# Kernel tuning notes

Measured on AMD Instinct MI355X. Metric: run time of the kernel, lower is better.

The kernel has to match this reference:

```python
import jax, jax.numpy as jnp
import numpy as np

GAMMA = 0.99


def setup_inputs() -> dict:
    key = jax.random.key(0)
    ks = jax.random.split(key, 6)
    T, D, H = 65536, 1024, 1024
    s1 = 1.0 / np.sqrt(D)
    s2 = 1.0 / np.sqrt(H)
    return {
        "rewards": jax.random.normal(ks[0], (T,), jnp.float32),
        "obs": jax.random.normal(ks[1], (T, D), jnp.float32),
        "W1": jax.random.normal(ks[2], (D, H), jnp.float32) * s1,
        "b1": jnp.zeros((H,), jnp.float32),
        "W2": jax.random.normal(ks[3], (H, H), jnp.float32) * s2,
        "b2": jnp.zeros((H,), jnp.float32),
        "W3": jax.random.normal(ks[4], (H, 1), jnp.float32) * s2,
        "b3": jnp.zeros((1,), jnp.float32),
    }


def _discounted_returns(rewards):
    # G[i] = r[i] + gamma * G[i+1], computed as a reverse scan
    def step(g, r):
        g = r + GAMMA * g
        return g, g
    _, G = jax.lax.scan(step, jnp.zeros((), rewards.dtype), rewards, reverse=True)
    return G


def reference(rewards, obs, W1, b1, W2, b2, W3, b3):
    G = _discounted_returns(rewards)              # [T]
    h = jax.nn.relu(obs @ W1 + b1)                # [T, H]
    h = jax.nn.relu(h @ W2 + b2)                  # [T, H]
    V = (h @ W3 + b3).reshape(-1)                 # [T]
    return G - V
```

## Files before the change

kernel.cpp:

```cpp
#include <hip/hip_runtime.h>

typedef __bf16 bf16x8 __attribute__((ext_vector_type(8)));
typedef __bf16 bf16x4 __attribute__((ext_vector_type(4)));
typedef float  f32x4  __attribute__((ext_vector_type(4)));

#define GAMMA 0.99f

__device__ __forceinline__ void gload_lds16(const void* g, void* l) {
  __builtin_amdgcn_global_load_lds(
      (const __attribute__((address_space(1))) void*)g,
      (__attribute__((address_space(3))) void*)l, 16, 0, 0);
}

#define VMCNT(n) asm volatile("s_waitcnt vmcnt(" #n ")" ::: "memory")
#define BAR() __builtin_amdgcn_s_barrier()
#define MFMA(d, a, b) d = __builtin_amdgcn_mfma_f32_16x16x32_bf16(a, b, d, 0, 0, 0)

__global__ __launch_bounds__(1024) void prep(
    const float* __restrict__ rw, float* __restrict__ G,
    const float* __restrict__ W1, const float* __restrict__ W2,
    __bf16* __restrict__ BT1, __bf16* __restrict__ BT2) {
  __shared__ float smem[4224];
  const int blk = blockIdx.x;
  const int t = threadIdx.x;
  if (blk == 0) {
    float* sv = smem;
    const float4* rp = (const float4*)(rw + t * 64);
    float4 lv[16];
#pragma unroll
    for (int i = 0; i < 16; ++i) lv[i] = rp[i];
    float loc[64];
#pragma unroll
    for (int i = 0; i < 16; ++i) {
      loc[4 * i + 0] = lv[i].x; loc[4 * i + 1] = lv[i].y;
      loc[4 * i + 2] = lv[i].z; loc[4 * i + 3] = lv[i].w;
    }
    float g = 0.f;
#pragma unroll
    for (int j = 63; j >= 0; --j) { g = loc[j] + GAMMA * g; loc[j] = g; }
    sv[t] = g;
    float W = GAMMA;
#pragma unroll
    for (int i = 0; i < 6; ++i) W *= W;
    float v = g;
    for (int s = 1; s < 1024; s <<= 1) {
      __syncthreads();
      float o = (t + s < 1024) ? sv[t + s] : 0.f;
      __syncthreads();
      v += W * o;
      sv[t] = v;
      W *= W;
    }
    __syncthreads();
    const float nxt = (t < 1023) ? sv[t + 1] : 0.f;
    float pw = GAMMA;
#pragma unroll
    for (int j = 63; j >= 0; --j) {
      G[t * 64 + j] = loc[j] + pw * nxt;
      pw *= GAMMA;
    }
  } else {
    const int sub = t >> 8, tt = t & 255;
    const int wi = (blk - 1) * 4 + sub;
    const float* W = (wi >= 1024) ? W2 : W1;
    __bf16* O = (wi >= 1024) ? BT2 : BT1;
    const int tile = wi & 1023;
    const int ti = tile >> 5, tj = tile & 31;
    float* s = smem + sub * 1056;
    const int rr = tt >> 3, c4 = (tt & 7) * 4;
    float4 v = *(const float4*)(W + (size_t)(ti * 32 + rr) * 1024 + tj * 32 + c4);
    s[rr * 33 + c4 + 0] = v.x; s[rr * 33 + c4 + 1] = v.y;
    s[rr * 33 + c4 + 2] = v.z; s[rr * 33 + c4 + 3] = v.w;
    __syncthreads();
    bf16x4 o = {(__bf16)s[(c4 + 0) * 33 + rr], (__bf16)s[(c4 + 1) * 33 + rr],
                (__bf16)s[(c4 + 2) * 33 + rr], (__bf16)s[(c4 + 3) * 33 + rr]};
    *(bf16x4*)(O + (size_t)(tj * 32 + rr) * 1024 + ti * 32 + c4) = o;
  }
}

__global__ __launch_bounds__(512, 2) void gemm1(
    const float* __restrict__ obs, const __bf16* __restrict__ BT1,
    const float* __restrict__ b1, __bf16* __restrict__ h1) {
  extern __shared__ char lds[];
  const int t = threadIdx.x, lane = t & 63, w = t >> 6;
  const int wsr = w >> 2, wsc = w & 3, g = lane >> 4, l15 = lane & 15;
  const int bid = blockIdx.x;
  const int mb = (bid & 7) * 32 + ((bid >> 3) >> 2);
  const int nb = (bid >> 3) & 3;

  const size_t stg_off =
      (size_t)(t >> 2) * 2048 + (size_t)(((t & 3) ^ ((t >> 3) & 3)) * 16);
  const char* Bg = (const char*)BT1 + (size_t)nb * 524288 + stg_off;
  const char* Asrc = (const char*)obs +
      ((size_t)(mb * 256 + w * 32 + (lane >> 3)) * 4096) +
      (size_t)(16 * ((lane & 7) ^ (lane >> 3)));
  const int aldst = w * 4096 + lane * 16;

  const int csw = (g ^ ((l15 >> 1) & 3)) << 4;
  const int brb = (wsc * 32 + l15) * 64 + csw;

  f32x4 acc[2][4][2][2];
  const f32x4 zero = {0.f, 0.f, 0.f, 0.f};
#pragma unroll
  for (int a_ = 0; a_ < 2; ++a_)
#pragma unroll
    for (int b_ = 0; b_ < 4; ++b_)
#pragma unroll
      for (int c_ = 0; c_ < 2; ++c_)
#pragma unroll
        for (int d_ = 0; d_ < 2; ++d_) acc[a_][b_][c_][d_] = zero;

  auto STA = [&](int buf, int kt) {
    const char* s = Asrc + kt * 128;
    char* d = lds + buf * 49152 + aldst;
    gload_lds16(s, d);
    gload_lds16(s + 32768, d + 1024);
    gload_lds16(s + 65536, d + 2048);
    gload_lds16(s + 98304, d + 3072);
  };
  auto STB = [&](int buf, int kt) {
    const char* s = Bg + kt * 64;
    char* d = lds + buf * 49152 + 32768 + t * 16;
    gload_lds16(s, d);
    gload_lds16(s + 262144, d + 8192);
  };
  auto LDAF = [&](const char* ab, int r) -> bf16x8 {
    const int o1 = (g * 32) ^ ((r & 7) << 4);
    const f32x4 a0 = *(const f32x4*)(ab + r * 128 + o1);
    const f32x4 a1 = *(const f32x4*)(ab + r * 128 + (o1 ^ 16));
    bf16x8 v = {(__bf16)a0[0], (__bf16)a0[1], (__bf16)a0[2], (__bf16)a0[3],
                (__bf16)a1[0], (__bf16)a1[1], (__bf16)a1[2], (__bf16)a1[3]};
    return v;
  };
  auto COMPUTE = [&](int bc) {
    const char* ab = lds + bc * 49152;
    const char* bb = ab + 32768;
    bf16x8 bfr[2][2], afr[4];
#pragma unroll
    for (int nh = 0; nh < 2; ++nh)
#pragma unroll
      for (int j = 0; j < 2; ++j)
        bfr[nh][j] = *(const bf16x8*)(bb + brb + (nh * 128 + j * 16) * 64);
#pragma unroll
    for (int i = 0; i < 4; ++i) afr[i] = LDAF(ab, wsr * 64 + 16 * i + l15);
    __builtin_amdgcn_s_setprio(1);
#pragma unroll
    for (int i = 0; i < 4; ++i)
#pragma unroll
      for (int nh = 0; nh < 2; ++nh)
#pragma unroll
        for (int j = 0; j < 2; ++j)
          MFMA(acc[0][i][nh][j], bfr[nh][j], afr[i]);
    __builtin_amdgcn_s_setprio(0);
#pragma unroll
    for (int i = 0; i < 4; ++i)
      afr[i] = LDAF(ab, 128 + wsr * 64 + 16 * i + l15);
    __builtin_amdgcn_s_setprio(1);
#pragma unroll
    for (int i = 0; i < 4; ++i)
#pragma unroll
      for (int nh = 0; nh < 2; ++nh)
#pragma unroll
        for (int j = 0; j < 2; ++j)
          MFMA(acc[1][i][nh][j], bfr[nh][j], afr[i]);
    __builtin_amdgcn_s_setprio(0);
  };

  STA(0, 0); STB(0, 0);
  STA(1, 1); STB(1, 1);
  int bc = 0;
  for (int kt = 0; kt < 30; ++kt) {
    int bs = bc + 2; if (bs >= 3) bs -= 3;
    STA(bs, kt + 2);
    STB(bs, kt + 2);
    VMCNT(12);
    BAR();
    COMPUTE(bc);
    BAR();
    bc = bc + 1; if (bc >= 3) bc -= 3;
  }
  VMCNT(6);
  BAR();
  COMPUTE(bc);
  BAR();
  bc = bc + 1; if (bc >= 3) bc -= 3;
  VMCNT(0);
  BAR();
  COMPUTE(bc);

  f32x4 b1q[2][2];
#pragma unroll
  for (int nh = 0; nh < 2; ++nh)
#pragma unroll
    for (int j = 0; j < 2; ++j)
      b1q[nh][j] =
          *(const f32x4*)(b1 + nb * 256 + nh * 128 + wsc * 32 + j * 16 + g * 4);
#pragma unroll
  for (int mh = 0; mh < 2; ++mh)
#pragma unroll
    for (int i = 0; i < 4; ++i) {
      const size_t mrow = (size_t)(mb * 256 + mh * 128 + wsr * 64 + i * 16 + l15);
#pragma unroll
      for (int nh = 0; nh < 2; ++nh)
#pragma unroll
        for (int j = 0; j < 2; ++j) {
          f32x4 v = acc[mh][i][nh][j];
          v.x += b1q[nh][j].x; v.y += b1q[nh][j].y;
          v.z += b1q[nh][j].z; v.w += b1q[nh][j].w;
          v.x = v.x > 0.f ? v.x : 0.f;
          v.y = v.y > 0.f ? v.y : 0.f;
          v.z = v.z > 0.f ? v.z : 0.f;
          v.w = v.w > 0.f ? v.w : 0.f;
          bf16x4 o = {(__bf16)v.x, (__bf16)v.y, (__bf16)v.z, (__bf16)v.w};
          *(bf16x4*)(h1 + mrow * 1024 + nb * 256 + nh * 128 + wsc * 32 +
                     j * 16 + g * 4) = o;
        }
    }
}

__global__ __launch_bounds__(512, 2) void gemm2(
    const __bf16* __restrict__ h1, const __bf16* __restrict__ BT2,
    const float* __restrict__ b2, const float* __restrict__ W3,
    float* __restrict__ V4) {
  extern __shared__ char lds[];
  const int t = threadIdx.x, lane = t & 63, w = t >> 6;
  const int wsr = w >> 2, wsc = w & 3, g = lane >> 4, l15 = lane & 15;
  const int bid = blockIdx.x;
  const int mb = (bid & 7) * 32 + ((bid >> 3) >> 2);
  const int nb = (bid >> 3) & 3;
  const size_t stg_off =
      (size_t)(t >> 2) * 2048 + (size_t)(((t & 3) ^ ((t >> 3) & 3)) * 16);
  const char* Ag = (const char*)h1 + (size_t)mb * 524288 + stg_off;
  const char* Bg = (const char*)BT2 + (size_t)nb * 524288 + stg_off;
  const int csw = (g ^ ((l15 >> 1) & 3)) << 4;
  const int arb = (wsr * 64 + l15) * 64 + csw;
  const int brb = (wsc * 32 + l15) * 64 + csw + 16384;

  f32x4 acc[2][4][2][2];
  const f32x4 zero = {0.f, 0.f, 0.f, 0.f};
#pragma unroll
  for (int a_ = 0; a_ < 2; ++a_)
#pragma unroll
    for (int b_ = 0; b_ < 4; ++b_)
#pragma unroll
      for (int c_ = 0; c_ < 2; ++c_)
#pragma unroll
        for (int d_ = 0; d_ < 2; ++d_) acc[a_][b_][c_][d_] = zero;

  auto STA = [&](int buf, int kt) {
    const char* s = Ag + kt * 64;
    char* d = lds + buf * 32768 + t * 16;
    gload_lds16(s, d);
    gload_lds16(s + 262144, d + 8192);
  };
  auto STB = [&](int buf, int kt) {
    const char* s = Bg + kt * 64;
    char* d = lds + buf * 32768 + 16384 + t * 16;
    gload_lds16(s, d);
    gload_lds16(s + 262144, d + 8192);
  };
  auto COMPUTE = [&](int bc) {
    const char* ab = lds + bc * 32768;
    bf16x8 bfr[2][2], afr[4];
#pragma unroll
    for (int nh = 0; nh < 2; ++nh)
#pragma unroll
      for (int j = 0; j < 2; ++j)
        bfr[nh][j] = *(const bf16x8*)(ab + brb + (nh * 128 + j * 16) * 64);
#pragma unroll
    for (int i = 0; i < 4; ++i)
      afr[i] = *(const bf16x8*)(ab + arb + (i * 16) * 64);
    __builtin_amdgcn_s_setprio(1);
#pragma unroll
    for (int i = 0; i < 4; ++i)
#pragma unroll
      for (int nh = 0; nh < 2; ++nh)
#pragma unroll
        for (int j = 0; j < 2; ++j)
          MFMA(acc[0][i][nh][j], bfr[nh][j], afr[i]);
    __builtin_amdgcn_s_setprio(0);
#pragma unroll
    for (int i = 0; i < 4; ++i)
      afr[i] = *(const bf16x8*)(ab + arb + ((128 + i * 16) * 64));
    __builtin_amdgcn_s_setprio(1);
#pragma unroll
    for (int i = 0; i < 4; ++i)
#pragma unroll
      for (int nh = 0; nh < 2; ++nh)
#pragma unroll
        for (int j = 0; j < 2; ++j)
          MFMA(acc[1][i][nh][j], bfr[nh][j], afr[i]);
    __builtin_amdgcn_s_setprio(0);
  };

  STA(0, 0); STB(0, 0);
  STA(1, 1); STB(1, 1);
  STA(2, 2); STB(2, 2);
  int bc = 0;
  for (int kt = 0; kt < 29; ++kt) {
    int bs = bc + 3; if (bs >= 4) bs -= 4;
    STA(bs, kt + 3);
    STB(bs, kt + 3);
    VMCNT(12);
    BAR();
    COMPUTE(bc);
    BAR();
    bc = (bc + 1) & 3;
  }
  VMCNT(8);
  BAR();
  COMPUTE(bc);
  BAR();
  bc = (bc + 1) & 3;
  VMCNT(4);
  BAR();
  COMPUTE(bc);
  BAR();
  bc = (bc + 1) & 3;
  VMCNT(0);
  BAR();
  COMPUTE(bc);

  f32x4 b2q[2][2], w3q[2][2];
#pragma unroll
  for (int nh = 0; nh < 2; ++nh)
#pragma unroll
    for (int j = 0; j < 2; ++j) {
      const int C = nb * 256 + nh * 128 + wsc * 32 + j * 16 + g * 4;
      b2q[nh][j] = *(const f32x4*)(b2 + C);
      w3q[nh][j] = *(const f32x4*)(W3 + C);
    }
  float p[2][4];
#pragma unroll
  for (int mh = 0; mh < 2; ++mh)
#pragma unroll
    for (int i = 0; i < 4; ++i) {
      float s = 0.f;
#pragma unroll
      for (int nh = 0; nh < 2; ++nh)
#pragma unroll
        for (int j = 0; j < 2; ++j) {
          f32x4 v = acc[mh][i][nh][j];
          v.x += b2q[nh][j].x; v.y += b2q[nh][j].y;
          v.z += b2q[nh][j].z; v.w += b2q[nh][j].w;
          v.x = v.x > 0.f ? v.x : 0.f;
          v.y = v.y > 0.f ? v.y : 0.f;
          v.z = v.z > 0.f ? v.z : 0.f;
          v.w = v.w > 0.f ? v.w : 0.f;
          s += v.x * w3q[nh][j].x + v.y * w3q[nh][j].y +
               v.z * w3q[nh][j].z + v.w * w3q[nh][j].w;
        }
      p[mh][i] = s;
    }
#pragma unroll
  for (int mh = 0; mh < 2; ++mh)
#pragma unroll
    for (int i = 0; i < 4; ++i) {
      p[mh][i] += __shfl_xor(p[mh][i], 16, 64);
      p[mh][i] += __shfl_xor(p[mh][i], 32, 64);
    }
  float* vp = (float*)lds;
  if (g == 0) {
#pragma unroll
    for (int mh = 0; mh < 2; ++mh)
#pragma unroll
      for (int i = 0; i < 4; ++i)
        vp[wsc * 256 + mh * 128 + wsr * 64 + i * 16 + l15] = p[mh][i];
  }
  __syncthreads();
  if (t < 256) {
    float s = vp[t] + vp[256 + t] + vp[512 + t] + vp[768 + t];
    V4[(size_t)nb * 65536 + mb * 256 + t] = s;
  }
}

__global__ __launch_bounds__(256) void final_kernel(const float* __restrict__ G,
                                                    const float* __restrict__ V4,
                                                    const float* __restrict__ b3,
                                                    float* __restrict__ out) {
  int i = blockIdx.x * 256 + threadIdx.x;
  out[i] = G[i] - (V4[i] + V4[65536 + i] + V4[131072 + i] + V4[196608 + i] + b3[0]);
}

extern "C" void kernel_launch(void* const* d_in, const int* in_sizes, int n_in,
                              void* d_out, int out_size, void* d_ws, size_t ws_size,
                              hipStream_t stream) {
  const float* rewards = (const float*)d_in[0];
  const float* obs = (const float*)d_in[1];
  const float* W1 = (const float*)d_in[2];
  const float* b1 = (const float*)d_in[3];
  const float* W2 = (const float*)d_in[4];
  const float* b2 = (const float*)d_in[5];
  const float* W3 = (const float*)d_in[6];
  const float* b3 = (const float*)d_in[7];
  float* out = (float*)d_out;

  char* ws = (char*)d_ws;
  __bf16* BT1 = (__bf16*)(ws);
  __bf16* BT2 = (__bf16*)(ws + (2u << 20));
  float* V4 = (float*)(ws + (4u << 20));
  float* G = (float*)(ws + (5u << 20));
  __bf16* h1 = (__bf16*)(ws + (8u << 20));

  hipFuncSetAttribute((const void*)gemm1,
                      hipFuncAttributeMaxDynamicSharedMemorySize, 147456);
  hipFuncSetAttribute((const void*)gemm2,
                      hipFuncAttributeMaxDynamicSharedMemorySize, 131072);

  prep<<<513, 1024, 0, stream>>>(rewards, G, W1, W2, BT1, BT2);
  gemm1<<<1024, 512, 147456, stream>>>(obs, BT1, b1, h1);
  gemm2<<<1024, 512, 131072, stream>>>(h1, BT2, b2, W3, V4);
  final_kernel<<<256, 256, 0, stream>>>(G, V4, b3, out);
}
```

Measured before the change: 370.5 us.

## Pre-convert obs to bf16 in prep kernel and shrink gemm1 tile

Adds a pass in the prep kernel that converts the fp32 obs matrix to bf16 in workspace with nontemporal loads and stores. gemm1 then stages bf16 A tiles directly, with no per-fragment fp32-to-bf16 conversion from LDS. Its M tile drops from 256 to 128 rows, which halves LDS use and doubles the grid. The cost is an extra 256MB read plus 128MB write round trip through HBM, and gemm1 now re-reads B for twice as many M tiles.

```diff
diff --git a/kernel.cpp b/kernel.cpp
--- a/kernel.cpp
+++ b/kernel.cpp
@@ -3,6 +3,8 @@
 typedef __bf16 bf16x8 __attribute__((ext_vector_type(8)));
 typedef __bf16 bf16x4 __attribute__((ext_vector_type(4)));
 typedef float  f32x4  __attribute__((ext_vector_type(4)));
+typedef unsigned long long u64;
+typedef unsigned long long u64x2 __attribute__((ext_vector_type(2)));
 
 #define GAMMA 0.99f
 
@@ -16,8 +18,9 @@
 #define BAR() __builtin_amdgcn_s_barrier()
 #define MFMA(d, a, b) d = __builtin_amdgcn_mfma_f32_16x16x32_bf16(a, b, d, 0, 0, 0)
 
-__global__ __launch_bounds__(1024) void prep(
+__global__ __launch_bounds__(1024) void mega_prep(
     const float* __restrict__ rw, float* __restrict__ G,
+    const float* __restrict__ obs, __bf16* __restrict__ obsb,
     const float* __restrict__ W1, const float* __restrict__ W2,
     __bf16* __restrict__ BT1, __bf16* __restrict__ BT2) {
   __shared__ float smem[4224];
@@ -59,9 +62,23 @@
       G[t * 64 + j] = loc[j] + pw * nxt;
       pw *= GAMMA;
     }
+  } else if (blk <= 2048) {
+    const size_t base = (size_t)(blk - 1) * 32768 + (size_t)t * 8;
+#pragma unroll
+    for (int it = 0; it < 4; ++it) {
+      const size_t e = base + (size_t)it * 8192;
+      const f32x4* p = (const f32x4*)(obs + e);
+      f32x4 u0 = __builtin_nontemporal_load(p);
+      f32x4 u1 = __builtin_nontemporal_load(p + 1);
+      bf16x8 o = {(__bf16)u0[0], (__bf16)u0[1], (__bf16)u0[2], (__bf16)u0[3],
+                  (__bf16)u1[0], (__bf16)u1[1], (__bf16)u1[2], (__bf16)u1[3]};
+      union { bf16x8 v; u64x2 u; } cv;
+      cv.v = o;
+      __builtin_nontemporal_store(cv.u, (u64x2*)(obsb + e));
+    }
   } else {
     const int sub = t >> 8, tt = t & 255;
-    const int wi = (blk - 1) * 4 + sub;
+    const int wi = (blk - 2049) * 4 + sub;
     const float* W = (wi >= 1024) ? W2 : W1;
     __bf16* O = (wi >= 1024) ? BT2 : BT1;
     const int tile = wi & 1023;
@@ -79,70 +96,51 @@
 }
 
 __global__ __launch_bounds__(512, 2) void gemm1(
-    const float* __restrict__ obs, const __bf16* __restrict__ BT1,
+    const __bf16* __restrict__ obsb, const __bf16* __restrict__ BT1,
     const float* __restrict__ b1, __bf16* __restrict__ h1) {
   extern __shared__ char lds[];
   const int t = threadIdx.x, lane = t & 63, w = t >> 6;
   const int wsr = w >> 2, wsc = w & 3, g = lane >> 4, l15 = lane & 15;
   const int bid = blockIdx.x;
-  const int mb = (bid & 7) * 32 + ((bid >> 3) >> 2);
+  const int mb = (bid & 7) * 64 + (bid >> 5);
   const int nb = (bid >> 3) & 3;
-
-  const size_t stg_off =
-      (size_t)(t >> 2) * 2048 + (size_t)(((t & 3) ^ ((t >> 3) & 3)) * 16);
-  const char* Bg = (const char*)BT1 + (size_t)nb * 524288 + stg_off;
-  const char* Asrc = (const char*)obs +
-      ((size_t)(mb * 256 + w * 32 + (lane >> 3)) * 4096) +
-      (size_t)(16 * ((lane & 7) ^ (lane >> 3)));
-  const int aldst = w * 4096 + lane * 16;
-
+  const size_t stg = (size_t)(t >> 2) * 2048 +
+                     (size_t)(((t & 3) ^ ((t >> 3) & 3)) * 16);
+  const char* Ag = (const char*)obsb + (size_t)mb * 262144 + stg;
+  const char* Bg = (const char*)BT1 + (size_t)nb * 524288 + stg;
   const int csw = (g ^ ((l15 >> 1) & 3)) << 4;
-  const int brb = (wsc * 32 + l15) * 64 + csw;
-
-  f32x4 acc[2][4][2][2];
+  const int arb = (wsr * 64 + l15) * 64 + csw;
+  const int brb = (wsc * 32 + l15) * 64 + csw + 8192;
+
+  f32x4 acc[4][2][2];
   const f32x4 zero = {0.f, 0.f, 0.f, 0.f};
 #pragma unroll
-  for (int a_ = 0; a_ < 2; ++a_)
-#pragma unroll
-    for (int b_ = 0; b_ < 4; ++b_)
-#pragma unroll
-      for (int c_ = 0; c_ < 2; ++c_)
-#pragma unroll
-        for (int d_ = 0; d_ < 2; ++d_) acc[a_][b_][c_][d_] = zero;
+  for (int i = 0; i < 4; ++i)
+#pragma unroll
+    for (int c_ = 0; c_ < 2; ++c_)
+#pragma unroll
+      for (int d_ = 0; d_ < 2; ++d_) acc[i][c_][d_] = zero;
 
   auto STA = [&](int buf, int kt) {
-    const char* s = Asrc + kt * 128;
-    char* d = lds + buf * 49152 + aldst;
-    gload_lds16(s, d);
-    gload_lds16(s + 32768, d + 1024);
-    gload_lds16(s + 65536, d + 2048);
-    gload_lds16(s + 98304, d + 3072);
+    gload_lds16(Ag + kt * 64, lds + buf * 24576 + t * 16);
   };
   auto STB = [&](int buf, int kt) {
     const char* s = Bg + kt * 64;
-    char* d = lds + buf * 49152 + 32768 + t * 16;
+    char* d = lds + buf * 24576 + 8192 + t * 16;
     gload_lds16(s, d);
     gload_lds16(s + 262144, d + 8192);
   };
-  auto LDAF = [&](const char* ab, int r) -> bf16x8 {
-    const int o1 = (g * 32) ^ ((r & 7) << 4);
-    const f32x4 a0 = *(const f32x4*)(ab + r * 128 + o1);
-    const f32x4 a1 = *(const f32x4*)(ab + r * 128 + (o1 ^ 16));
-    bf16x8 v = {(__bf16)a0[0], (__bf16)a0[1], (__bf16)a0[2], (__bf16)a0[3],
-                (__bf16)a1[0], (__bf16)a1[1], (__bf16)a1[2], (__bf16)a1[3]};
-    return v;
-  };
   auto COMPUTE = [&](int bc) {
-    const char* ab = lds + bc * 49152;
-    const char* bb = ab + 32768;
+    const char* ab = lds + bc * 24576;
     bf16x8 bfr[2][2], afr[4];
 #pragma unroll
     for (int nh = 0; nh < 2; ++nh)
 #pragma unroll
       for (int j = 0; j < 2; ++j)
-        bfr[nh][j] = *(const bf16x8*)(bb + brb + (nh * 128 + j * 16) * 64);
-#pragma unroll
-    for (int i = 0; i < 4; ++i) afr[i] = LDAF(ab, wsr * 64 + 16 * i + l15);
+        bfr[nh][j] = *(const bf16x8*)(ab + brb + (nh * 128 + j * 16) * 64);
+#pragma unroll
+    for (int i = 0; i < 4; ++i)
+      afr[i] = *(const bf16x8*)(ab + arb + (i * 16) * 64);
     __builtin_amdgcn_s_setprio(1);
 #pragma unroll
     for (int i = 0; i < 4; ++i)
@@ -150,19 +148,7 @@
       for (int nh = 0; nh < 2; ++nh)
 #pragma unroll
         for (int j = 0; j < 2; ++j)
-          MFMA(acc[0][i][nh][j], bfr[nh][j], afr[i]);
-    __builtin_amdgcn_s_setprio(0);
-#pragma unroll
-    for (int i = 0; i < 4; ++i)
-      afr[i] = LDAF(ab, 128 + wsr * 64 + 16 * i + l15);
-    __builtin_amdgcn_s_setprio(1);
-#pragma unroll
-    for (int i = 0; i < 4; ++i)
-#pragma unroll
-      for (int nh = 0; nh < 2; ++nh)
-#pragma unroll
-        for (int j = 0; j < 2; ++j)
-          MFMA(acc[1][i][nh][j], bfr[nh][j], afr[i]);
+          MFMA(acc[i][nh][j], bfr[nh][j], afr[i]);
     __builtin_amdgcn_s_setprio(0);
   };
 
@@ -173,13 +159,13 @@
     int bs = bc + 2; if (bs >= 3) bs -= 3;
     STA(bs, kt + 2);
     STB(bs, kt + 2);
-    VMCNT(12);
+    VMCNT(6);
     BAR();
     COMPUTE(bc);
     BAR();
     bc = bc + 1; if (bc >= 3) bc -= 3;
   }
-  VMCNT(6);
+  VMCNT(3);
   BAR();
   COMPUTE(bc);
   BAR();
@@ -196,26 +182,24 @@
       b1q[nh][j] =
           *(const f32x4*)(b1 + nb * 256 + nh * 128 + wsc * 32 + j * 16 + g * 4);
 #pragma unroll
-  for (int mh = 0; mh < 2; ++mh)
-#pragma unroll
-    for (int i = 0; i < 4; ++i) {
-      const size_t mrow = (size_t)(mb * 256 + mh * 128 + wsr * 64 + i * 16 + l15);
-#pragma unroll
-      for (int nh = 0; nh < 2; ++nh)
-#pragma unroll
-        for (int j = 0; j < 2; ++j) {
-          f32x4 v = acc[mh][i][nh][j];
-          v.x += b1q[nh][j].x; v.y += b1q[nh][j].y;
-          v.z += b1q[nh][j].z; v.w += b1q[nh][j].w;
-          v.x = v.x > 0.f ? v.x : 0.f;
-          v.y = v.y > 0.f ? v.y : 0.f;
-          v.z = v.z > 0.f ? v.z : 0.f;
-          v.w = v.w > 0.f ? v.w : 0.f;
-          bf16x4 o = {(__bf16)v.x, (__bf16)v.y, (__bf16)v.z, (__bf16)v.w};
-          *(bf16x4*)(h1 + mrow * 1024 + nb * 256 + nh * 128 + wsc * 32 +
-                     j * 16 + g * 4) = o;
-        }
-    }
+  for (int i = 0; i < 4; ++i) {
+    const size_t mrow = (size_t)(mb * 128 + wsr * 64 + i * 16 + l15);
+#pragma unroll
+    for (int nh = 0; nh < 2; ++nh)
+#pragma unroll
+      for (int j = 0; j < 2; ++j) {
+        f32x4 v = acc[i][nh][j];
+        v.x += b1q[nh][j].x; v.y += b1q[nh][j].y;
+        v.z += b1q[nh][j].z; v.w += b1q[nh][j].w;
+        v.x = v.x > 0.f ? v.x : 0.f;
+        v.y = v.y > 0.f ? v.y : 0.f;
+        v.z = v.z > 0.f ? v.z : 0.f;
+        v.w = v.w > 0.f ? v.w : 0.f;
+        bf16x4 o = {(__bf16)v.x, (__bf16)v.y, (__bf16)v.z, (__bf16)v.w};
+        *(bf16x4*)(h1 + mrow * 1024 + nb * 256 + nh * 128 + wsc * 32 +
+                   j * 16 + g * 4) = o;
+      }
+  }
 }
 
 __global__ __launch_bounds__(512, 2) void gemm2(
@@ -400,15 +384,16 @@
   __bf16* BT2 = (__bf16*)(ws + (2u << 20));
   float* V4 = (float*)(ws + (4u << 20));
   float* G = (float*)(ws + (5u << 20));
-  __bf16* h1 = (__bf16*)(ws + (8u << 20));
+  __bf16* obsb = (__bf16*)(ws + (8u << 20));
+  __bf16* h1 = (__bf16*)(ws + (136u << 20));
 
   hipFuncSetAttribute((const void*)gemm1,
-                      hipFuncAttributeMaxDynamicSharedMemorySize, 147456);
+                      hipFuncAttributeMaxDynamicSharedMemorySize, 73728);
   hipFuncSetAttribute((const void*)gemm2,
                       hipFuncAttributeMaxDynamicSharedMemorySize, 131072);
 
-  prep<<<513, 1024, 0, stream>>>(rewards, G, W1, W2, BT1, BT2);
-  gemm1<<<1024, 512, 147456, stream>>>(obs, BT1, b1, h1);
+  mega_prep<<<2561, 1024, 0, stream>>>(rewards, G, obs, obsb, W1, W2, BT1, BT2);
+  gemm1<<<2048, 512, 73728, stream>>>(obsb, BT1, b1, h1);
   gemm2<<<1024, 512, 131072, stream>>>(h1, BT2, b2, W3, V4);
   final_kernel<<<256, 256, 0, stream>>>(G, V4, b3, out);
 }
```

After: 386.0 us. 1.04x slower.
